# Performance work log

Measured on AMD Instinct MI355X. Metric: run time of the kernel, lower is better.

The kernel has to match this reference:

```python
import jax, jax.numpy as jnp
import numpy as np

KERNEL_SIZE = 2
DILATION = 2


def aconv(x, A, shift):
    # x: [n, c, v, l], A: [v, w]; temporal roll + zero-mask first `shift` steps,
    # then node diffusion x . A over the node axis.
    xr = jnp.roll(x, shift, axis=3)
    if shift > 0:
        xr = xr.at[..., :shift].set(0.0)
    return jnp.einsum('ncvl,vw->ncwl', xr, A)


def setup_inputs() -> dict:
    key = jax.random.key(0)
    ks = jax.random.split(key, 7)
    N, C, V, L, E, CO = 32, 64, 500, 64, 10, 64
    return {
        'x': jax.random.normal(ks[0], (N, C, V, L), dtype=jnp.float32),
        'nodevec1': jax.random.normal(ks[1], (V, E), dtype=jnp.float32),
        'nodevec2': jax.random.normal(ks[2], (E, V), dtype=jnp.float32),
        'et_w': jax.random.normal(ks[3], (E, E), dtype=jnp.float32),
        'et_b': jax.random.normal(ks[4], (E,), dtype=jnp.float32),
        'mlp_w': jax.random.normal(ks[5], (CO, (1 + KERNEL_SIZE) * C), dtype=jnp.float32) * 0.05,
        'mlp_b': jax.random.normal(ks[6], (CO,), dtype=jnp.float32),
    }


def reference(x, nodevec1, nodevec2, et_w, et_b, mlp_w, mlp_b):
    out = [x]
    x2 = x
    shift = 0
    # hop 0: adaptive adjacency from node embeddings
    adp = jax.nn.softmax(jax.nn.relu(nodevec1 @ nodevec2), axis=1)
    x1 = aconv(x2, adp, shift)
    out.append(x1)
    shift = DILATION
    x2 = x1
    for i in range(KERNEL_SIZE - 1):
        # emb_trans: affine update of both node embeddings
        nodevec1 = nodevec1 @ et_w + et_b
        nodevec2 = (nodevec2.T @ et_w + et_b).T
        adp = jax.nn.softmax(jax.nn.relu(nodevec1 @ nodevec2), axis=1)
        x1 = aconv(x2, adp, shift)
        out.append(x1)
        shift = shift + DILATION
        x2 = x1
    h = jnp.concatenate(out, axis=1)  # [n, (1+K)*c, v, l]
    # 1x1 conv == channel matmul; dropout is identity at inference
    h = jnp.einsum('ncvl,oc->novl', h, mlp_w) + mlp_b[None, :, None, None]
    return h
```

## Files before the change

kernel.cpp:

```cpp
#include <hip/hip_runtime.h>
#include <hip/hip_bf16.h>

#define NB 32
#define CC 64
#define VV 500
#define LL 64
#define EE 10
#define CO 64
#define DIL 2
#define VP 512
#define SL (VV * LL)

typedef unsigned short u16;
typedef unsigned int   u32;
typedef __attribute__((ext_vector_type(8))) short bf16x8;
typedef __attribute__((ext_vector_type(4))) float f32x4;

typedef const __attribute__((address_space(1))) void g_void;
typedef __attribute__((address_space(3))) void l_void;

__device__ __forceinline__ float bf2f(u16 u) {
    union { u32 i; float f; } c; c.i = ((u32)u) << 16; return c.f;
}
__device__ __forceinline__ u16 f2bf(float f) {
    union { float f; u32 i; } c; c.f = f;
    u32 x = c.i;
    u32 r = (x + 0x7fffu + ((x >> 16) & 1u)) >> 16;
    return (u16)r;
}

__global__ void emb_kernel(const float* __restrict__ nv1, const float* __restrict__ nv2,
                           const float* __restrict__ et_w, const float* __restrict__ et_b,
                           const float* __restrict__ mlp_w,
                           float* __restrict__ nv1t, float* __restrict__ nv2t,
                           u16* __restrict__ wb) {
    int idx = blockIdx.x * blockDim.x + threadIdx.x;
    if (idx < VV * EE) {
        int v = idx / EE, e = idx - v * EE;
        float s = et_b[e];
        #pragma unroll
        for (int f = 0; f < EE; f++) s += nv1[v * EE + f] * et_w[f * EE + e];
        nv1t[idx] = s;
    } else if (idx < 2 * VV * EE) {
        int k = idx - VV * EE;
        int e = k / VV, v = k - e * VV;
        float s = et_b[e];
        #pragma unroll
        for (int f = 0; f < EE; f++) s += nv2[f * VV + v] * et_w[f * EE + e];
        nv2t[k] = s;
    } else if (idx < 2 * VV * EE + CO * 3 * CC) {
        int k = idx - 2 * VV * EE;
        wb[k] = f2bf(mlp_w[k]);
    }
}

__global__ __launch_bounds__(64) void adj_kernel(const float* __restrict__ p1,
                                                 const float* __restrict__ p2,
                                                 u16* __restrict__ Atb) {
    const int v = blockIdx.x;
    const int lane = threadIdx.x;
    if (v >= VV) {
        #pragma unroll
        for (int j = 0; j < 8; j++) Atb[(size_t)(lane + 64 * j) * VP + v] = 0;
        return;
    }
    float e1[EE];
    #pragma unroll
    for (int e = 0; e < EE; e++) e1[e] = p1[v * EE + e];

    float r[8];
    float m = -1e30f;
    #pragma unroll
    for (int j = 0; j < 8; j++) {
        int w = lane + 64 * j;
        if (w < VV) {
            float s = 0.f;
            #pragma unroll
            for (int e = 0; e < EE; e++) s += e1[e] * p2[e * VV + w];
            r[j] = fmaxf(s, 0.f);
            m = fmaxf(m, r[j]);
        } else {
            r[j] = -1e30f;
        }
    }
    #pragma unroll
    for (int off = 32; off > 0; off >>= 1) m = fmaxf(m, __shfl_xor(m, off));

    float p[8];
    float sum = 0.f;
    #pragma unroll
    for (int j = 0; j < 8; j++) {
        int w = lane + 64 * j;
        if (w < VV) { p[j] = expf(r[j] - m); sum += p[j]; }
    }
    #pragma unroll
    for (int off = 32; off > 0; off >>= 1) sum += __shfl_xor(sum, off);
    float inv = 1.f / sum;
    #pragma unroll
    for (int j = 0; j < 8; j++) {
        int w = lane + 64 * j;
        Atb[(size_t)w * VP + v] = (w < VV) ? f2bf(p[j] * inv) : (u16)0;
    }
}

__global__ __launch_bounds__(512, 2) void hops_fused(const float* __restrict__ x,
                                                     const u16* __restrict__ Atb0,
                                                     const u16* __restrict__ Atb1,
                                                     u16* __restrict__ x1g,
                                                     u16* __restrict__ x2g) {
    __shared__ u16 Xt[LL * VP];
    __shared__ u16 Ab[8][3][64 * 32];
    const int nc = blockIdx.x;
    const int tid = threadIdx.x;
    const size_t base = (size_t)nc * (VV * LL);
    const int lane = tid & 63;
    const int wv = tid >> 6;
    const int wr = wv * 64;

    int growoff[4];
    #pragma unroll
    for (int j = 0; j < 4; ++j) {
        const int lin = j * 1024 + lane * 16;
        const int wl = lin >> 6;
        const int cell = ((lin >> 4) & 3) ^ ((wl >> 1) & 3);
        growoff[j] = (wr + wl) * VP + cell * 8;
    }
    char* mybuf[3];
    #pragma unroll
    for (int k = 0; k < 3; ++k) mybuf[k] = (char*)&Ab[wv][k][0];

    auto issue_chunk = [&](const u16* Asrc, int kb, char* dst) {
        #pragma unroll
        for (int j = 0; j < 4; ++j)
            __builtin_amdgcn_global_load_lds(
                (g_void*)(Asrc + growoff[j] + kb),
                (l_void*)(dst + j * 1024 + lane * 16), 16, 0, 0);
    };

    issue_chunk(Atb0, 0, mybuf[0]);
    issue_chunk(Atb0, 32, mybuf[1]);

    {
        char* ldsb = (char*)Xt;
        const int lquad = lane & 15;
        const int vsub = lane >> 4;
        const int l0 = 4 * lquad;
        #pragma unroll
        for (int i = 0; i < 8; ++i) {
            const int vp = wv * 32 + i * 4 + vsub;
            const int v0 = 2 * vp;
            u32 pk0, pk1, pk2, pk3;
            if (v0 < VV) {
                const float* xa = x + base + v0 * LL + l0;
                float4 fa = *(const float4*)xa;
                float4 fb = *(const float4*)(xa + LL);
                pk0 = (u32)f2bf(fa.x) | ((u32)f2bf(fb.x) << 16);
                pk1 = (u32)f2bf(fa.y) | ((u32)f2bf(fb.y) << 16);
                pk2 = (u32)f2bf(fa.z) | ((u32)f2bf(fb.z) << 16);
                pk3 = (u32)f2bf(fa.w) | ((u32)f2bf(fb.w) << 16);
            } else {
                pk0 = pk1 = pk2 = pk3 = 0;
            }
            const int vb = 4 * vp;
            int l = l0;
            *(u32*)(ldsb + l * (VP * 2) + (vb ^ ((l & 7) << 4))) = pk0; l++;
            *(u32*)(ldsb + l * (VP * 2) + (vb ^ ((l & 7) << 4))) = pk1; l++;
            *(u32*)(ldsb + l * (VP * 2) + (vb ^ ((l & 7) << 4))) = pk2; l++;
            *(u32*)(ldsb + l * (VP * 2) + (vb ^ ((l & 7) << 4))) = pk3;
        }
    }
    __syncthreads();

    const int r15 = lane & 15;
    const int kg = lane >> 4;
    const char* ldsb = (const char*)Xt;
    int lrow[4], lswz[4], aoff[4];
    #pragma unroll
    for (int ct = 0; ct < 4; ct++) {
        const int l = ct * 16 + r15;
        lrow[ct] = l * (VP * 2);
        lswz[ct] = (l & 7) << 4;
    }
    #pragma unroll
    for (int rt = 0; rt < 4; rt++) {
        const int wl = rt * 16 + r15;
        aoff[rt] = wl * 64 + ((kg ^ ((wl >> 1) & 3)) << 4);
    }

    f32x4 acc[4][4];
    #pragma unroll
    for (int rt = 0; rt < 4; rt++)
        #pragma unroll
        for (int ct = 0; ct < 4; ct++)
            acc[rt][ct] = (f32x4){0.f, 0.f, 0.f, 0.f};

    #pragma unroll
    for (int s = 0; s < 16; ++s) {
        asm volatile("s_waitcnt vmcnt(4) lgkmcnt(0)" ::: "memory");
        const int g1 = s + 2;
        issue_chunk(g1 < 16 ? Atb0 : Atb1, (g1 & 15) * 32, mybuf[g1 % 3]);

        const char* ac = mybuf[s % 3];
        bf16x8 a[4], b[4];
        #pragma unroll
        for (int rt = 0; rt < 4; rt++)
            a[rt] = *(const bf16x8*)(ac + aoff[rt]);
        #pragma unroll
        for (int ct = 0; ct < 4; ct++)
            b[ct] = *(const bf16x8*)(ldsb + lrow[ct] + ((s * 64 + kg * 16) ^ lswz[ct]));
        #pragma unroll
        for (int rt = 0; rt < 4; rt++)
            #pragma unroll
            for (int ct = 0; ct < 4; ct++)
                acc[rt][ct] = __builtin_amdgcn_mfma_f32_16x16x32_bf16(a[rt], b[ct], acc[rt][ct], 0, 0, 0);
    }

    {
        u16* xo = x1g + base;
        #pragma unroll
        for (int rt = 0; rt < 4; rt++) {
            #pragma unroll
            for (int ct = 0; ct < 4; ct++) {
                const int col = ct * 16 + r15;
                const int wbase = wr + rt * 16 + kg * 4;
                f32x4 c = acc[rt][ct];
                #pragma unroll
                for (int r = 0; r < 4; r++) {
                    int w = wbase + r;
                    if (w < VV) xo[w * LL + col] = f2bf(c[r]);
                }
            }
        }
    }
    __syncthreads();
    {
        char* ldsw = (char*)Xt;
        {
            const int l = tid >> 8;
            const int j = tid & 255;
            *(u32*)(ldsw + l * (VP * 2) + 4 * j) = 0;
        }
        #pragma unroll
        for (int rt = 0; rt < 4; rt++) {
            const int wb2 = (wr + rt * 16 + kg * 4) * 2;
            #pragma unroll
            for (int ct = 0; ct < 4; ct++) {
                const int col = ct * 16 + r15;
                const int ln = col + DIL;
                if (ln < LL) {
                    f32x4 c = acc[rt][ct];
                    u32 plo = (u32)f2bf(c[0]) | ((u32)f2bf(c[1]) << 16);
                    u32 phi = (u32)f2bf(c[2]) | ((u32)f2bf(c[3]) << 16);
                    const int swz = (ln & 7) << 4;
                    char* p = ldsw + ln * (VP * 2);
                    *(u32*)(p + (wb2 ^ swz)) = plo;
                    *(u32*)(p + ((wb2 + 4) ^ swz)) = phi;
                }
            }
        }
    }
    __syncthreads();

    #pragma unroll
    for (int rt = 0; rt < 4; rt++)
        #pragma unroll
        for (int ct = 0; ct < 4; ct++)
            acc[rt][ct] = (f32x4){0.f, 0.f, 0.f, 0.f};

    #pragma unroll
    for (int s = 16; s < 32; ++s) {
        if (s == 31) {
            asm volatile("s_waitcnt vmcnt(0) lgkmcnt(0)" ::: "memory");
        } else {
            asm volatile("s_waitcnt vmcnt(4) lgkmcnt(0)" ::: "memory");
        }
        const int g1 = s + 2;
        if (g1 < 32)
            issue_chunk(Atb1, (g1 & 15) * 32, mybuf[g1 % 3]);

        const char* ac = mybuf[s % 3];
        const int kk = s - 16;
        bf16x8 a[4], b[4];
        #pragma unroll
        for (int rt = 0; rt < 4; rt++)
            a[rt] = *(const bf16x8*)(ac + aoff[rt]);
        #pragma unroll
        for (int ct = 0; ct < 4; ct++)
            b[ct] = *(const bf16x8*)(ldsb + lrow[ct] + ((kk * 64 + kg * 16) ^ lswz[ct]));
        #pragma unroll
        for (int rt = 0; rt < 4; rt++)
            #pragma unroll
            for (int ct = 0; ct < 4; ct++)
                acc[rt][ct] = __builtin_amdgcn_mfma_f32_16x16x32_bf16(a[rt], b[ct], acc[rt][ct], 0, 0, 0);
    }

    {
        u16* xo = x2g + base;
        #pragma unroll
        for (int rt = 0; rt < 4; rt++) {
            #pragma unroll
            for (int ct = 0; ct < 4; ct++) {
                const int col = ct * 16 + r15;
                const int wbase = wr + rt * 16 + kg * 4;
                f32x4 c = acc[rt][ct];
                #pragma unroll
                for (int r = 0; r < 4; r++) {
                    int w = wbase + r;
                    if (w < VV) xo[w * LL + col] = f2bf(c[r]);
                }
            }
        }
    }
}

__global__ __launch_bounds__(256, 3) void mlp_mfma(const float* __restrict__ x,
                                                   const u16* __restrict__ x1,
                                                   const u16* __restrict__ x2,
                                                   const u16* __restrict__ wb,
                                                   const float* __restrict__ b,
                                                   float* __restrict__ out) {
    __shared__ u16 Ht[128 * 192];
    const int bid = blockIdx.x;
    const int n = bid / (SL / 128);
    const int st = bid - n * (SL / 128);
    const int s0 = st * 128;
    const int tid = threadIdx.x;

    const int lane = tid & 63;
    const int wv = tid >> 6;
    const int obase = (wv & 1) * 32;
    const int sbase = (wv >> 1) * 64;
    const int r15 = lane & 15;
    const int kg = lane >> 4;

    bf16x8 afrag[2][6];
    #pragma unroll
    for (int rt = 0; rt < 2; rt++)
        #pragma unroll
        for (int ks = 0; ks < 6; ks++)
            afrag[rt][ks] = *(const bf16x8*)(wb + (obase + rt * 16 + r15) * (3 * CC) + ks * 32 + kg * 8);

    {
        char* ldsb = (char*)Ht;
        const int squad = tid >> 3;
        const int pgroup = tid & 7;
        const int sq0 = 4 * squad;
        #pragma unroll
        for (int i = 0; i < 12; ++i) {
            const int P = i * 8 + pgroup;
            const int c = 2 * P;
            u32 pk0, pk1, pk2, pk3;
            if (i < 4) {
                const float* fsrc = x + ((size_t)n * CC + c) * SL + s0 + sq0;
                float4 va = *(const float4*)fsrc;
                float4 vb = *(const float4*)(fsrc + SL);
                pk0 = (u32)f2bf(va.x) | ((u32)f2bf(vb.x) << 16);
                pk1 = (u32)f2bf(va.y) | ((u32)f2bf(vb.y) << 16);
                pk2 = (u32)f2bf(va.z) | ((u32)f2bf(vb.z) << 16);
                pk3 = (u32)f2bf(va.w) | ((u32)f2bf(vb.w) << 16);
            } else {
                const u16* bsrc = (i < 8)
                    ? x1 + ((size_t)n * CC + (c - CC)) * SL + s0 + sq0
                    : x2 + ((size_t)n * CC + (c - 2 * CC)) * SL + s0 + sq0;
                uint2 va = *(const uint2*)bsrc;
                uint2 vb = *(const uint2*)(bsrc + SL);
                pk0 = (va.x & 0xffffu) | (vb.x << 16);
                pk1 = (va.x >> 16) | (vb.x & 0xffff0000u);
                pk2 = (va.y & 0xffffu) | (vb.y << 16);
                pk3 = (va.y >> 16) | (vb.y & 0xffff0000u);
            }
            int s = sq0;
            *(u32*)(ldsb + s * 384 + ((4 * P) ^ ((s & 7) << 4))) = pk0; s++;
            *(u32*)(ldsb + s * 384 + ((4 * P) ^ ((s & 7) << 4))) = pk1; s++;
            *(u32*)(ldsb + s * 384 + ((4 * P) ^ ((s & 7) << 4))) = pk2; s++;
            *(u32*)(ldsb + s * 384 + ((4 * P) ^ ((s & 7) << 4))) = pk3;
        }
    }
    __syncthreads();

    f32x4 acc[2][4];
    #pragma unroll
    for (int rt = 0; rt < 2; rt++)
        #pragma unroll
        for (int ct = 0; ct < 4; ct++)
            acc[rt][ct] = (f32x4){0.f, 0.f, 0.f, 0.f};

    const char* ldsb = (const char*)Ht;
    #pragma unroll
    for (int ks = 0; ks < 6; ks++) {
        bf16x8 bfr[4];
        #pragma unroll
        for (int ct = 0; ct < 4; ct++) {
            const int s = sbase + ct * 16 + r15;
            bfr[ct] = *(const bf16x8*)(ldsb + s * 384 + ((ks * 64 + kg * 16) ^ ((s & 7) << 4)));
        }
        #pragma unroll
        for (int rt = 0; rt < 2; rt++)
            #pragma unroll
            for (int ct = 0; ct < 4; ct++)
                acc[rt][ct] = __builtin_amdgcn_mfma_f32_16x16x32_bf16(afrag[rt][ks], bfr[ct], acc[rt][ct], 0, 0, 0);
    }

    #pragma unroll
    for (int rt = 0; rt < 2; rt++) {
        #pragma unroll
        for (int r = 0; r < 4; r++) {
            const int o = obase + rt * 16 + kg * 4 + r;
            const float bias = b[o];
            float* orow = out + ((size_t)n * CO + o) * SL + s0 + sbase;
            #pragma unroll
            for (int ct = 0; ct < 4; ct++)
                orow[ct * 16 + r15] = acc[rt][ct][r] + bias;
        }
    }
}

extern "C" void kernel_launch(void* const* d_in, const int* in_sizes, int n_in,
                              void* d_out, int out_size, void* d_ws, size_t ws_size,
                              hipStream_t stream) {
    const float* x     = (const float*)d_in[0];
    const float* nv1   = (const float*)d_in[1];
    const float* nv2   = (const float*)d_in[2];
    const float* et_w  = (const float*)d_in[3];
    const float* et_b  = (const float*)d_in[4];
    const float* mlp_w = (const float*)d_in[5];
    const float* mlp_b = (const float*)d_in[6];
    float* out = (float*)d_out;

    char* wsb = (char*)d_ws;
    size_t off = 0;
    auto alloc = [&](size_t bytes) {
        size_t o = off;
        off += (bytes + 255) & ~(size_t)255;
        return o;
    };
    u16*   Atb0 = (u16*)(wsb + alloc((size_t)VP * VP * 2));
    u16*   Atb1 = (u16*)(wsb + alloc((size_t)VP * VP * 2));
    float* nv1t = (float*)(wsb + alloc((size_t)VV * EE * 4));
    float* nv2t = (float*)(wsb + alloc((size_t)EE * VV * 4));
    u16*   wb   = (u16*)(wsb + alloc((size_t)CO * 3 * CC * 2));
    u16*   x1   = (u16*)(wsb + alloc((size_t)NB * CC * VV * LL * 2));
    u16*   x2   = (u16*)(wsb + alloc((size_t)NB * CC * VV * LL * 2));
    (void)in_sizes; (void)n_in; (void)out_size; (void)ws_size;

    const int embN = 2 * VV * EE + CO * 3 * CC;
    emb_kernel<<<(embN + 255) / 256, 256, 0, stream>>>(nv1, nv2, et_w, et_b, mlp_w, nv1t, nv2t, wb);
    adj_kernel<<<VP, 64, 0, stream>>>(nv1, nv2, Atb0);
    adj_kernel<<<VP, 64, 0, stream>>>(nv1t, nv2t, Atb1);
    hops_fused<<<NB * CC, 512, 0, stream>>>(x, Atb0, Atb1, x1, x2);
    mlp_mfma<<<NB * (SL / 128), 256, 0, stream>>>(x, x1, x2, wb, mlp_b, out);
}
```

Before: 445.7 us.

## Software-pipeline LDS fragment loads in hop GEMMs and merge adjacency kernels

Restructures both MFMA loops in the fused hop kernel so the next step's A and B fragments are loaded from LDS while the current step's MFMAs run. Wraps the MFMA block in s_setprio to favour the math wave. The two adjacency-build launches are merged into a single grid covering both matrices. This hides LDS latency and saves one launch, but double-buffering the fragments raises register pressure and the waitcnt ordering is now hand-managed.

Result: no change. 440.3 us (-1.2%).

```diff
diff --git a/kernel.cpp b/kernel.cpp
--- a/kernel.cpp
+++ b/kernel.cpp
@@ -54,10 +54,17 @@
     }
 }
 
-__global__ __launch_bounds__(64) void adj_kernel(const float* __restrict__ p1,
-                                                 const float* __restrict__ p2,
-                                                 u16* __restrict__ Atb) {
-    const int v = blockIdx.x;
+__global__ __launch_bounds__(64) void adj2_kernel(const float* __restrict__ nv1,
+                                                  const float* __restrict__ nv2,
+                                                  const float* __restrict__ nv1t,
+                                                  const float* __restrict__ nv2t,
+                                                  u16* __restrict__ Atb0,
+                                                  u16* __restrict__ Atb1) {
+    const int which = blockIdx.x >> 9;
+    const int v = blockIdx.x & (VP - 1);
+    const float* p1 = which ? nv1t : nv1;
+    const float* p2 = which ? nv2t : nv2;
+    u16* Atb = which ? Atb1 : Atb0;
     const int lane = threadIdx.x;
     if (v >= VV) {
         #pragma unroll
@@ -194,26 +201,44 @@
         for (int ct = 0; ct < 4; ct++)
             acc[rt][ct] = (f32x4){0.f, 0.f, 0.f, 0.f};
 
-    #pragma unroll
-    for (int s = 0; s < 16; ++s) {
-        asm volatile("s_waitcnt vmcnt(4) lgkmcnt(0)" ::: "memory");
+    bf16x8 a[4], b[4], an[4], bn[4];
+
+    #pragma unroll
+    for (int rt = 0; rt < 4; rt++) a[rt] = *(const bf16x8*)(mybuf[0] + aoff[rt]);
+    #pragma unroll
+    for (int ct = 0; ct < 4; ct++) b[ct] = *(const bf16x8*)(ldsb + lrow[ct] + ((kg * 16) ^ lswz[ct]));
+
+    #pragma unroll
+    for (int s = 0; s < 15; ++s) {
+        #pragma unroll
+        for (int ct = 0; ct < 4; ct++)
+            bn[ct] = *(const bf16x8*)(ldsb + lrow[ct] + (((s + 1) * 64 + kg * 16) ^ lswz[ct]));
         const int g1 = s + 2;
         issue_chunk(g1 < 16 ? Atb0 : Atb1, (g1 & 15) * 32, mybuf[g1 % 3]);
-
-        const char* ac = mybuf[s % 3];
-        bf16x8 a[4], b[4];
+        asm volatile("s_waitcnt vmcnt(4)" ::: "memory");
         #pragma unroll
         for (int rt = 0; rt < 4; rt++)
-            a[rt] = *(const bf16x8*)(ac + aoff[rt]);
-        #pragma unroll
-        for (int ct = 0; ct < 4; ct++)
-            b[ct] = *(const bf16x8*)(ldsb + lrow[ct] + ((s * 64 + kg * 16) ^ lswz[ct]));
+            an[rt] = *(const bf16x8*)(mybuf[(s + 1) % 3] + aoff[rt]);
+        __builtin_amdgcn_s_setprio(1);
         #pragma unroll
         for (int rt = 0; rt < 4; rt++)
             #pragma unroll
             for (int ct = 0; ct < 4; ct++)
                 acc[rt][ct] = __builtin_amdgcn_mfma_f32_16x16x32_bf16(a[rt], b[ct], acc[rt][ct], 0, 0, 0);
-    }
+        __builtin_amdgcn_s_setprio(0);
+        #pragma unroll
+        for (int rt = 0; rt < 4; rt++) a[rt] = an[rt];
+        #pragma unroll
+        for (int ct = 0; ct < 4; ct++) b[ct] = bn[ct];
+    }
+    issue_chunk(Atb1, 32, mybuf[17 % 3]);
+    __builtin_amdgcn_s_setprio(1);
+    #pragma unroll
+    for (int rt = 0; rt < 4; rt++)
+        #pragma unroll
+        for (int ct = 0; ct < 4; ct++)
+            acc[rt][ct] = __builtin_amdgcn_mfma_f32_16x16x32_bf16(a[rt], b[ct], acc[rt][ct], 0, 0, 0);
+    __builtin_amdgcn_s_setprio(0);
 
     {
         u16* xo = x1g + base;
@@ -268,31 +293,46 @@
             acc[rt][ct] = (f32x4){0.f, 0.f, 0.f, 0.f};
 
     #pragma unroll
-    for (int s = 16; s < 32; ++s) {
-        if (s == 31) {
-            asm volatile("s_waitcnt vmcnt(0) lgkmcnt(0)" ::: "memory");
-        } else {
-            asm volatile("s_waitcnt vmcnt(4) lgkmcnt(0)" ::: "memory");
-        }
+    for (int rt = 0; rt < 4; rt++) a[rt] = *(const bf16x8*)(mybuf[16 % 3] + aoff[rt]);
+    #pragma unroll
+    for (int ct = 0; ct < 4; ct++) b[ct] = *(const bf16x8*)(ldsb + lrow[ct] + ((kg * 16) ^ lswz[ct]));
+
+    #pragma unroll
+    for (int s = 16; s < 31; ++s) {
+        const int kk1 = s - 16 + 1;
+        #pragma unroll
+        for (int ct = 0; ct < 4; ct++)
+            bn[ct] = *(const bf16x8*)(ldsb + lrow[ct] + ((kk1 * 64 + kg * 16) ^ lswz[ct]));
         const int g1 = s + 2;
         if (g1 < 32)
             issue_chunk(Atb1, (g1 & 15) * 32, mybuf[g1 % 3]);
-
-        const char* ac = mybuf[s % 3];
-        const int kk = s - 16;
-        bf16x8 a[4], b[4];
+        if (s == 30) {
+            asm volatile("s_waitcnt vmcnt(0)" ::: "memory");
+        } else {
+            asm volatile("s_waitcnt vmcnt(4)" ::: "memory");
+        }
         #pragma unroll
         for (int rt = 0; rt < 4; rt++)
-            a[rt] = *(const bf16x8*)(ac + aoff[rt]);
-        #pragma unroll
-        for (int ct = 0; ct < 4; ct++)
-            b[ct] = *(const bf16x8*)(ldsb + lrow[ct] + ((kk * 64 + kg * 16) ^ lswz[ct]));
+            an[rt] = *(const bf16x8*)(mybuf[(s + 1) % 3] + aoff[rt]);
+        __builtin_amdgcn_s_setprio(1);
         #pragma unroll
         for (int rt = 0; rt < 4; rt++)
             #pragma unroll
             for (int ct = 0; ct < 4; ct++)
                 acc[rt][ct] = __builtin_amdgcn_mfma_f32_16x16x32_bf16(a[rt], b[ct], acc[rt][ct], 0, 0, 0);
-    }
+        __builtin_amdgcn_s_setprio(0);
+        #pragma unroll
+        for (int rt = 0; rt < 4; rt++) a[rt] = an[rt];
+        #pragma unroll
+        for (int ct = 0; ct < 4; ct++) b[ct] = bn[ct];
+    }
+    __builtin_amdgcn_s_setprio(1);
+    #pragma unroll
+    for (int rt = 0; rt < 4; rt++)
+        #pragma unroll
+        for (int ct = 0; ct < 4; ct++)
+            acc[rt][ct] = __builtin_amdgcn_mfma_f32_16x16x32_bf16(a[rt], b[ct], acc[rt][ct], 0, 0, 0);
+    __builtin_amdgcn_s_setprio(0);
 
     {
         u16* xo = x2g + base;
@@ -445,8 +485,7 @@
 
     const int embN = 2 * VV * EE + CO * 3 * CC;
     emb_kernel<<<(embN + 255) / 256, 256, 0, stream>>>(nv1, nv2, et_w, et_b, mlp_w, nv1t, nv2t, wb);
-    adj_kernel<<<VP, 64, 0, stream>>>(nv1, nv2, Atb0);
-    adj_kernel<<<VP, 64, 0, stream>>>(nv1t, nv2t, Atb1);
+    adj2_kernel<<<2 * VP, 64, 0, stream>>>(nv1, nv2, nv1t, nv2t, Atb0, Atb1);
     hops_fused<<<NB * CC, 512, 0, stream>>>(x, Atb0, Atb1, x1, x2);
     mlp_mfma<<<NB * (SL / 128), 256, 0, stream>>>(x, x1, x2, wb, mlp_b, out);
 }
```

## Split hop GEMM across 16 waves per block and merge adjacency launches

Applied to the files above, without the earlier changes.

Each (n,c) block now uses 1024 threads (16 waves), each wave owning 32 output rows instead of 64. This halves the per-wave accumulators and A-chunk loads, and the wait counts are adjusted to match. MFMA sections are wrapped in s_setprio to favour matrix issue, and the two adjacency kernel launches are merged into one grid. The aim is more latency hiding and less register pressure per wave. The trade-off is that each wave's B-operand LDS reads are now amortised over half as many MFMAs, and LDS use per block stays large at roughly 64KB Xt plus 96KB of A buffers.

Measured after the change: 427.5 us. 4.1% less time.

```diff
diff --git a/kernel.cpp b/kernel.cpp
--- a/kernel.cpp
+++ b/kernel.cpp
@@ -54,10 +54,17 @@
     }
 }
 
-__global__ __launch_bounds__(64) void adj_kernel(const float* __restrict__ p1,
-                                                 const float* __restrict__ p2,
-                                                 u16* __restrict__ Atb) {
-    const int v = blockIdx.x;
+__global__ __launch_bounds__(64) void adj2_kernel(const float* __restrict__ nv1,
+                                                  const float* __restrict__ nv2,
+                                                  const float* __restrict__ nv1t,
+                                                  const float* __restrict__ nv2t,
+                                                  u16* __restrict__ Atb0,
+                                                  u16* __restrict__ Atb1) {
+    const int which = blockIdx.x >> 9;
+    const int v = blockIdx.x & (VP - 1);
+    const float* p1 = which ? nv1t : nv1;
+    const float* p2 = which ? nv2t : nv2;
+    u16* Atb = which ? Atb1 : Atb0;
     const int lane = threadIdx.x;
     if (v >= VV) {
         #pragma unroll
@@ -103,26 +110,26 @@
     }
 }
 
-__global__ __launch_bounds__(512, 2) void hops_fused(const float* __restrict__ x,
-                                                     const u16* __restrict__ Atb0,
-                                                     const u16* __restrict__ Atb1,
-                                                     u16* __restrict__ x1g,
-                                                     u16* __restrict__ x2g) {
+__global__ __launch_bounds__(1024, 4) void hops_fused(const float* __restrict__ x,
+                                                      const u16* __restrict__ Atb0,
+                                                      const u16* __restrict__ Atb1,
+                                                      u16* __restrict__ x1g,
+                                                      u16* __restrict__ x2g) {
     __shared__ u16 Xt[LL * VP];
-    __shared__ u16 Ab[8][3][64 * 32];
-    const int nc = blockIdx.x;
+    __shared__ u16 Ab[16][3][32 * 32];
     const int tid = threadIdx.x;
-    const size_t base = (size_t)nc * (VV * LL);
     const int lane = tid & 63;
     const int wv = tid >> 6;
-    const int wr = wv * 64;
-
-    int growoff[4];
-    #pragma unroll
-    for (int j = 0; j < 4; ++j) {
+    const int wr = wv * 32;
+    const size_t base = (size_t)blockIdx.x * (VV * LL);
+
+    int growoff[2], ldsoff[2];
+    #pragma unroll
+    for (int j = 0; j < 2; ++j) {
         const int lin = j * 1024 + lane * 16;
         const int wl = lin >> 6;
         const int cell = ((lin >> 4) & 3) ^ ((wl >> 1) & 3);
+        ldsoff[j] = lin;
         growoff[j] = (wr + wl) * VP + cell * 8;
     }
     char* mybuf[3];
@@ -131,10 +138,10 @@
 
     auto issue_chunk = [&](const u16* Asrc, int kb, char* dst) {
         #pragma unroll
-        for (int j = 0; j < 4; ++j)
+        for (int j = 0; j < 2; ++j)
             __builtin_amdgcn_global_load_lds(
                 (g_void*)(Asrc + growoff[j] + kb),
-                (l_void*)(dst + j * 1024 + lane * 16), 16, 0, 0);
+                (l_void*)(dst + ldsoff[j]), 16, 0, 0);
     };
 
     issue_chunk(Atb0, 0, mybuf[0]);
@@ -146,8 +153,8 @@
         const int vsub = lane >> 4;
         const int l0 = 4 * lquad;
         #pragma unroll
-        for (int i = 0; i < 8; ++i) {
-            const int vp = wv * 32 + i * 4 + vsub;
+        for (int i = 0; i < 4; ++i) {
+            const int vp = wv * 16 + i * 4 + vsub;
             const int v0 = 2 * vp;
             u32 pk0, pk1, pk2, pk3;
             if (v0 < VV) {
@@ -174,7 +181,7 @@
     const int r15 = lane & 15;
     const int kg = lane >> 4;
     const char* ldsb = (const char*)Xt;
-    int lrow[4], lswz[4], aoff[4];
+    int lrow[4], lswz[4], aoff[2];
     #pragma unroll
     for (int ct = 0; ct < 4; ct++) {
         const int l = ct * 16 + r15;
@@ -182,43 +189,45 @@
         lswz[ct] = (l & 7) << 4;
     }
     #pragma unroll
-    for (int rt = 0; rt < 4; rt++) {
+    for (int rt = 0; rt < 2; rt++) {
         const int wl = rt * 16 + r15;
         aoff[rt] = wl * 64 + ((kg ^ ((wl >> 1) & 3)) << 4);
     }
 
-    f32x4 acc[4][4];
-    #pragma unroll
-    for (int rt = 0; rt < 4; rt++)
+    f32x4 acc[2][4];
+    #pragma unroll
+    for (int rt = 0; rt < 2; rt++)
         #pragma unroll
         for (int ct = 0; ct < 4; ct++)
             acc[rt][ct] = (f32x4){0.f, 0.f, 0.f, 0.f};
 
     #pragma unroll
     for (int s = 0; s < 16; ++s) {
-        asm volatile("s_waitcnt vmcnt(4) lgkmcnt(0)" ::: "memory");
+        asm volatile("s_waitcnt vmcnt(2) lgkmcnt(0)" ::: "memory");
         const int g1 = s + 2;
         issue_chunk(g1 < 16 ? Atb0 : Atb1, (g1 & 15) * 32, mybuf[g1 % 3]);
 
         const char* ac = mybuf[s % 3];
-        bf16x8 a[4], b[4];
-        #pragma unroll
-        for (int rt = 0; rt < 4; rt++)
+        bf16x8 a[2], b[4];
+        #pragma unroll
+        for (int rt = 0; rt < 2; rt++)
             a[rt] = *(const bf16x8*)(ac + aoff[rt]);
         #pragma unroll
         for (int ct = 0; ct < 4; ct++)
             b[ct] = *(const bf16x8*)(ldsb + lrow[ct] + ((s * 64 + kg * 16) ^ lswz[ct]));
-        #pragma unroll
-        for (int rt = 0; rt < 4; rt++)
+        __builtin_amdgcn_s_setprio(1);
+        #pragma unroll
+        for (int rt = 0; rt < 2; rt++)
             #pragma unroll
             for (int ct = 0; ct < 4; ct++)
                 acc[rt][ct] = __builtin_amdgcn_mfma_f32_16x16x32_bf16(a[rt], b[ct], acc[rt][ct], 0, 0, 0);
+        __builtin_amdgcn_s_setprio(0);
     }
 
     {
         u16* xo = x1g + base;
         #pragma unroll
-        for (int rt = 0; rt < 4; rt++) {
+        for (int rt = 0; rt < 2; rt++) {
             #pragma unroll
             for (int ct = 0; ct < 4; ct++) {
                 const int col = ct * 16 + r15;
@@ -235,13 +244,13 @@
     __syncthreads();
     {
         char* ldsw = (char*)Xt;
-        {
+        if (tid < 512) {
             const int l = tid >> 8;
             const int j = tid & 255;
             *(u32*)(ldsw + l * (VP * 2) + 4 * j) = 0;
         }
         #pragma unroll
-        for (int rt = 0; rt < 4; rt++) {
+        for (int rt = 0; rt < 2; rt++) {
             const int wb2 = (wr + rt * 16 + kg * 4) * 2;
             #pragma unroll
             for (int ct = 0; ct < 4; ct++) {
@@ -262,7 +271,7 @@
     __syncthreads();
 
     #pragma unroll
-    for (int rt = 0; rt < 4; rt++)
+    for (int rt = 0; rt < 2; rt++)
         #pragma unroll
         for (int ct = 0; ct < 4; ct++)
             acc[rt][ct] = (f32x4){0.f, 0.f, 0.f, 0.f};
@@ -272,7 +281,7 @@
         if (s == 31) {
             asm volatile("s_waitcnt vmcnt(0) lgkmcnt(0)" ::: "memory");
         } else {
-            asm volatile("s_waitcnt vmcnt(4) lgkmcnt(0)" ::: "memory");
+            asm volatile("s_waitcnt vmcnt(2) lgkmcnt(0)" ::: "memory");
         }
         const int g1 = s + 2;
         if (g1 < 32)
@@ -280,24 +289,26 @@
 
         const char* ac = mybuf[s % 3];
         const int kk = s - 16;
-        bf16x8 a[4], b[4];
-        #pragma unroll
-        for (int rt = 0; rt < 4; rt++)
+        bf16x8 a[2], b[4];
+        #pragma unroll
+        for (int rt = 0; rt < 2; rt++)
             a[rt] = *(const bf16x8*)(ac + aoff[rt]);
         #pragma unroll
         for (int ct = 0; ct < 4; ct++)
             b[ct] = *(const bf16x8*)(ldsb + lrow[ct] + ((kk * 64 + kg * 16) ^ lswz[ct]));
-        #pragma unroll
-        for (int rt = 0; rt < 4; rt++)
+        __builtin_amdgcn_s_setprio(1);
+        #pragma unroll
+        for (int rt = 0; rt < 2; rt++)
             #pragma unroll
             for (int ct = 0; ct < 4; ct++)
                 acc[rt][ct] = __builtin_amdgcn_mfma_f32_16x16x32_bf16(a[rt], b[ct], acc[rt][ct], 0, 0, 0);
+        __builtin_amdgcn_s_setprio(0);
     }
 
     {
         u16* xo = x2g + base;
         #pragma unroll
-        for (int rt = 0; rt < 4; rt++) {
+        for (int rt = 0; rt < 2; rt++) {
             #pragma unroll
             for (int ct = 0; ct < 4; ct++) {
                 const int col = ct * 16 + r15;
@@ -445,8 +456,7 @@
 
     const int embN = 2 * VV * EE + CO * 3 * CC;
     emb_kernel<<<(embN + 255) / 256, 256, 0, stream>>>(nv1, nv2, et_w, et_b, mlp_w, nv1t, nv2t, wb);
-    adj_kernel<<<VP, 64, 0, stream>>>(nv1, nv2, Atb0);
-    adj_kernel<<<VP, 64, 0, stream>>>(nv1t, nv2t, Atb1);
-    hops_fused<<<NB * CC, 512, 0, stream>>>(x, Atb0, Atb1, x1, x2);
+    adj2_kernel<<<2 * VP, 64, 0, stream>>>(nv1, nv2, nv1t, nv2t, Atb0, Atb1);
+    hops_fused<<<NB * CC, 1024, 0, stream>>>(x, Atb0, Atb1, x1, x2);
     mlp_mfma<<<NB * (SL / 128), 256, 0, stream>>>(x, x1, x2, wb, mlp_b, out);
 }
```
